# Performance work log

Hardware: AMD Instinct MI355X
Metric: run time of the kernel (lower is better)

Reference implementation:

```python
import jax, jax.numpy as jnp
import numpy as np
from jax import lax

K = 33  # avgpool kernel
P = 16  # padding
EPS = 1e-08


def _box_sum(x):
    # Sum over 33x33 windows, stride 1, zero padding 16 on H and W (NCHW).
    return lax.reduce_window(
        x, 0.0, lax.add,
        window_dimensions=(1, 1, K, K),
        window_strides=(1, 1, 1, 1),
        padding=((0, 0), (0, 0), (P, P), (P, P)),
    )


def setup_inputs() -> dict:
    key = jax.random.key(0)
    input_tensor = jax.random.normal(key, (64, 1, 80, 3000), dtype=jnp.float32)
    return {"input_tensor": input_tensor}


def reference(input_tensor):
    B, C, H, W = input_tensor.shape
    # count_include_pad=False: divide by number of VALID elements per window.
    counts = _box_sum(jnp.ones((1, 1, H, W), dtype=input_tensor.dtype))
    local_mean = _box_sum(input_tensor) / counts
    centered = input_tensor - local_mean
    local_var = _box_sum(centered * centered) / counts
    local_std = jnp.sqrt(local_var)
    return centered / (local_std + EPS)
```

## Files before the change

kernel.cpp:

```cpp
#include <hip/hip_runtime.h>
#include <hip/hip_bf16.h>
#include <math.h>

#define BB 64
#define HH 80
#define WW 3000
#define RAD 16
#define TW 96
#define XSW 68
#define HXS 116
#define NSTRIP 32
#define NT 1024
#define EPSF 1e-8f

#define XS_WORDS (HH * XSW)
#define HXP_OFF  XS_WORDS
#define HXP_WORDS (TW * HXS)
#define ICH_OFF  (XS_WORDS + HXP_WORDS)
#define TOT_WORDS (ICH_OFF + HH)

typedef float f32x2 __attribute__((ext_vector_type(2)));
typedef float f32x4 __attribute__((ext_vector_type(4)));

__device__ __forceinline__ float bflo(uint32_t w) { return __uint_as_float(w << 16); }
__device__ __forceinline__ float bfhi(uint32_t w) { return __uint_as_float(w & 0xffff0000u); }
__device__ __forceinline__ uint32_t packbf2(float lo, float hi) {
    union { __hip_bfloat162 h2; uint32_t u; } u;
    u.h2 = __hip_bfloat162(__float2bfloat16(lo), __float2bfloat16(hi));
    return u.u;
}
__device__ __forceinline__ f32x2 uw(uint32_t w) {
    f32x2 r; r.x = bflo(w); r.y = bfhi(w); return r;
}

#define E4(V, J) ((J) == 0 ? (V).x : ((J) == 1 ? (V).y : ((J) == 2 ? (V).z : (V).w)))
#define W24(Q) E4((Q) < 4 ? v0 : (Q) < 8 ? v1 : (Q) < 12 ? v2 : (Q) < 16 ? v3 : (Q) < 20 ? v4 : v5, (Q) & 3)
#define W48(Q) E4((Q) < 4 ? R0 : (Q) < 8 ? R1 : (Q) < 12 ? R2 : (Q) < 16 ? R3 : (Q) < 20 ? R4 : \
                  (Q) < 24 ? R5 : (Q) < 28 ? R6 : (Q) < 32 ? R7 : (Q) < 36 ? R8 : \
                  (Q) < 40 ? R9 : (Q) < 44 ? R10 : R11, (Q) & 3)
#define F16(K) E4((K) < 4 ? f0 : (K) < 8 ? f1 : (K) < 12 ? f2 : f3, (K) & 3)

__global__ __launch_bounds__(NT, 8)
void localnorm_kernel(const float* __restrict__ in, float* __restrict__ out) {
    extern __shared__ uint32_t smem[];
    uint32_t* Hxp = smem + HXP_OFF;
    float* inv_ch = (float*)(smem + ICH_OFF);

    const int t     = threadIdx.x;
    const int strip = blockIdx.x % NSTRIP;
    const int b     = blockIdx.x / NSTRIP;
    const int c0    = strip * TW;

    if (t < HH) {
        int lo = max(t - RAD, 0), hi = min(t + RAD, HH - 1);
        inv_ch[t] = 1.0f / (float)(hi - lo + 1);
    }
    if (t < 768) {
        const int col = t >> 3;
        const int c8  = t & 7;
        const int off = col * HXS + ((c8 < 4) ? (c8 * 4) : (96 + (c8 - 4) * 4));
        *(uint4*)(Hxp + off) = make_uint4(0u, 0u, 0u, 0u);
    }

    {
        const float* inb = in + (size_t)b * (HH * WW);
        #pragma unroll
        for (int it = 0; it < 3; ++it) {
            const int id = t + it * NT;
            if (it < 2 || id < 2560) {
                const int row = id >> 5;
                const int q   = id & 31;
                const int gc  = c0 - 16 + 4 * q;
                uint2 w2;
                if (gc >= 0 && gc + 4 <= WW) {
                    float4 v = *(const float4*)(inb + (size_t)row * WW + gc);
                    w2.x = packbf2(v.x, v.y);
                    w2.y = packbf2(v.z, v.w);
                } else {
                    float p0 = (gc     >= 0 && gc     < WW) ? inb[(size_t)row * WW + gc]     : 0.f;
                    float p1 = (gc + 1 >= 0 && gc + 1 < WW) ? inb[(size_t)row * WW + gc + 1] : 0.f;
                    float p2 = (gc + 2 >= 0 && gc + 2 < WW) ? inb[(size_t)row * WW + gc + 2] : 0.f;
                    float p3 = (gc + 3 >= 0 && gc + 3 < WW) ? inb[(size_t)row * WW + gc + 3] : 0.f;
                    w2.x = packbf2(p0, p1);
                    w2.y = packbf2(p2, p3);
                }
                *(uint2*)(smem + row * XSW + 2 * q) = w2;
            }
        }
    }
    __syncthreads();

    {
        const int row = t % HH;
        const int s16 = t / HH;
        if (s16 < 6) {
            const uint32_t* xr = smem + row * XSW + s16 * 8;
            uint4 v0 = *(const uint4*)(xr);
            uint4 v1 = *(const uint4*)(xr + 4);
            uint4 v2 = *(const uint4*)(xr + 8);
            uint4 v3 = *(const uint4*)(xr + 12);
            uint4 v4 = *(const uint4*)(xr + 16);
            uint4 v5 = *(const uint4*)(xr + 20);
            float l16 = bflo(W24(16));
            f32x2 pA; pA.x = l16;       pA.y = 0.f;
            f32x2 qA; qA.x = l16 * l16; qA.y = 0.f;
            f32x2 pB; pB.x = 0.f; pB.y = 0.f;
            f32x2 qB; qB.x = 0.f; qB.y = 0.f;
            #pragma unroll
            for (int q = 0; q < 16; q += 2) {
                f32x2 uA = uw(W24(q));
                f32x2 uB = uw(W24(q + 1));
                pA += uA;      pB += uB;
                qA += uA * uA; qB += uB * uB;
            }
            f32x2 ps = pA + pB, qs = qA + qB;
            float ax  = ps.x + ps.y;
            float axx = qs.x + qs.y;
            uint32_t* hw = Hxp + (s16 * 16) * HXS + row + 16;
            #pragma unroll
            for (int k = 0; k < 8; ++k) {
                uint32_t wS = W24(k), wE = W24(k + 16);
                float lS = bflo(wS), hE = bfhi(wE);
                float a1x  = ax - lS + hE;
                float a1xx = axx - lS * lS + hE * hE;
                hw[(2 * k) * HXS]     = packbf2(ax, axx);
                hw[(2 * k + 1) * HXS] = packbf2(a1x, a1xx);
                if (k != 7) {
                    float hS = bfhi(wS), lN = bflo(W24(k + 17));
                    ax  = a1x - hS + lN;
                    axx = a1xx - hS * hS + lN * lN;
                }
            }
        }
    }
    __syncthreads();

    {
        const int c    = t % TW;
        const int band = t / TW;
        const int gc   = c0 + c;
        if (band < 5 && gc < WW) {
            const int r0 = band * 16;
            const uint32_t* hp = Hxp + c * HXS + r0;
            uint4 R0  = *(const uint4*)(hp);
            uint4 R1  = *(const uint4*)(hp + 4);
            uint4 R2  = *(const uint4*)(hp + 8);
            uint4 R3  = *(const uint4*)(hp + 12);
            uint4 R4  = *(const uint4*)(hp + 16);
            uint4 R5  = *(const uint4*)(hp + 20);
            uint4 R6  = *(const uint4*)(hp + 24);
            uint4 R7  = *(const uint4*)(hp + 28);
            uint4 R8  = *(const uint4*)(hp + 32);
            uint4 R9  = *(const uint4*)(hp + 36);
            uint4 R10 = *(const uint4*)(hp + 40);
            uint4 R11 = *(const uint4*)(hp + 44);
            f32x2 aA = uw(W48(32));
            f32x2 aB; aB.x = 0.f; aB.y = 0.f;
            #pragma unroll
            for (int q = 0; q < 32; q += 2) {
                aA += uw(W48(q));
                aB += uw(W48(q + 1));
            }
            f32x2 acc = aA + aB;
            const float icw = 1.0f / (float)(min(gc + RAD, WW - 1) - max(gc - RAD, 0) + 1);
            f32x4 f0 = *(const f32x4*)(inv_ch + r0);
            f32x4 f1 = *(const f32x4*)(inv_ch + r0 + 4);
            f32x4 f2 = *(const f32x4*)(inv_ch + r0 + 8);
            f32x4 f3 = *(const f32x4*)(inv_ch + r0 + 12);
            const int  xwoff  = (c + 16) >> 1;
            const bool hiHf   = ((c + 16) & 1) != 0;
            float* outb = out + (size_t)b * (HH * WW);
            #pragma unroll
            for (int k = 0; k < 16; ++k) {
                const int r = r0 + k;
                const float ninv = F16(k) * icw;
                f32x2 me = acc * ninv;
                float var = fmaxf(me.y - me.x * me.x, 1e-24f);
#if defined(__has_builtin) && __has_builtin(__builtin_amdgcn_rsqf)
                float isd = __builtin_amdgcn_rsqf(var);
#else
                float isd = __builtin_amdgcn_rcpf(__builtin_amdgcn_sqrtf(var) + EPSF);
#endif
                uint32_t xw = smem[r * XSW + xwoff];
                float xv = hiHf ? bfhi(xw) : bflo(xw);
                outb[(size_t)r * WW + gc] = (xv - me.x) * isd;
                if (k != 15) {
                    acc += uw(W48(k + 33)) - uw(W48(k));
                }
            }
        }
    }
}

extern "C" void kernel_launch(void* const* d_in, const int* in_sizes, int n_in,
                              void* d_out, int out_size, void* d_ws, size_t ws_size,
                              hipStream_t stream) {
    const float* in = (const float*)d_in[0];
    float* out = (float*)d_out;

    const size_t lds_bytes = (size_t)TOT_WORDS * sizeof(uint32_t);
    static bool attr_set = false;
    if (!attr_set) {
        (void)hipFuncSetAttribute((const void*)localnorm_kernel,
                                  hipFuncAttributeMaxDynamicSharedMemorySize,
                                  (int)lds_bytes);
        attr_set = true;
    }

    dim3 grid(BB * NSTRIP);
    dim3 block(NT);
    localnorm_kernel<<<grid, block, lds_bytes, stream>>>(in, out);
}
```

Measured before the change: 36.40 us.

## Stage input tile as fp32 via direct global-to-LDS loads with narrower strips

Input is now staged in LDS as fp32 rather than packed bf16, using the global_load_lds builtin so interior strips copy straight from global memory into LDS without passing through registers. The strip width drops from 96 to 80 columns (38 strips), and the horizontal pass is rewritten to work on fp32 values with FMA accumulation. The aim is to cut register round-trips and packing work in the load phase and to improve precision. The cost is a larger LDS footprint per block, more blocks overall, and extra halo reloads from the narrower strips.

```diff
diff --git a/kernel.cpp b/kernel.cpp
--- a/kernel.cpp
+++ b/kernel.cpp
@@ -6,10 +6,11 @@
 #define HH 80
 #define WW 3000
 #define RAD 16
-#define TW 96
-#define XSW 68
+#define TW 80
+#define NLOAD 112
+#define XSW 112
 #define HXS 116
-#define NSTRIP 32
+#define NSTRIP 38
 #define NT 1024
 #define EPSF 1e-8f
 
@@ -33,8 +34,21 @@
     f32x2 r; r.x = bflo(w); r.y = bfhi(w); return r;
 }
 
+#if defined(__has_builtin)
+#if __has_builtin(__builtin_amdgcn_global_load_lds)
+#define HAVE_GLL 1
+__device__ __forceinline__ void gload_lds16(const float* g, float* l) {
+    __builtin_amdgcn_global_load_lds(
+        (const __attribute__((address_space(1))) void*)g,
+        (__attribute__((address_space(3))) void*)l, 16, 0, 0);
+}
+#endif
+#endif
+
 #define E4(V, J) ((J) == 0 ? (V).x : ((J) == 1 ? (V).y : ((J) == 2 ? (V).z : (V).w)))
-#define W24(Q) E4((Q) < 4 ? v0 : (Q) < 8 ? v1 : (Q) < 12 ? v2 : (Q) < 16 ? v3 : (Q) < 20 ? v4 : v5, (Q) & 3)
+#define F48(Q) E4((Q) < 4 ? G0 : (Q) < 8 ? G1 : (Q) < 12 ? G2 : (Q) < 16 ? G3 : (Q) < 20 ? G4 : \
+                  (Q) < 24 ? G5 : (Q) < 28 ? G6 : (Q) < 32 ? G7 : (Q) < 36 ? G8 : \
+                  (Q) < 40 ? G9 : (Q) < 44 ? G10 : G11, (Q) & 3)
 #define W48(Q) E4((Q) < 4 ? R0 : (Q) < 8 ? R1 : (Q) < 12 ? R2 : (Q) < 16 ? R3 : (Q) < 20 ? R4 : \
                   (Q) < 24 ? R5 : (Q) < 28 ? R6 : (Q) < 32 ? R7 : (Q) < 36 ? R8 : \
                   (Q) < 40 ? R9 : (Q) < 44 ? R10 : R11, (Q) & 3)
@@ -43,48 +57,63 @@
 __global__ __launch_bounds__(NT, 8)
 void localnorm_kernel(const float* __restrict__ in, float* __restrict__ out) {
     extern __shared__ uint32_t smem[];
-    uint32_t* Hxp = smem + HXP_OFF;
-    float* inv_ch = (float*)(smem + ICH_OFF);
+    float*    smemf = (float*)smem;
+    uint32_t* Hxp   = smem + HXP_OFF;
+    float*   inv_ch = (float*)(smem + ICH_OFF);
 
     const int t     = threadIdx.x;
     const int strip = blockIdx.x % NSTRIP;
     const int b     = blockIdx.x / NSTRIP;
     const int c0    = strip * TW;
+    const float* inb = in + (size_t)b * (HH * WW);
 
     if (t < HH) {
         int lo = max(t - RAD, 0), hi = min(t + RAD, HH - 1);
         inv_ch[t] = 1.0f / (float)(hi - lo + 1);
     }
-    if (t < 768) {
+    if (t < 640) {
         const int col = t >> 3;
         const int c8  = t & 7;
         const int off = col * HXS + ((c8 < 4) ? (c8 * 4) : (96 + (c8 - 4) * 4));
         *(uint4*)(Hxp + off) = make_uint4(0u, 0u, 0u, 0u);
     }
 
-    {
-        const float* inb = in + (size_t)b * (HH * WW);
+    bool dma = false;
+#ifdef HAVE_GLL
+    dma = (c0 >= 16) && (c0 + NLOAD - 16 <= WW);
+#endif
+    if (dma) {
+#ifdef HAVE_GLL
+        const float* gsrc = inb + (c0 - 16);
+        #pragma unroll
+        for (int i = 0; i < 3; ++i) {
+            const int ck = t + i * NT;
+            if (i < 2 || ck < 2240) {
+                const int row = ck / 28;
+                const int m   = ck - row * 28;
+                gload_lds16(gsrc + (size_t)row * WW + 4 * m, smemf + 4 * ck);
+            }
+        }
+#endif
+    } else {
         #pragma unroll
         for (int it = 0; it < 3; ++it) {
             const int id = t + it * NT;
-            if (it < 2 || id < 2560) {
-                const int row = id >> 5;
-                const int q   = id & 31;
+            if (it < 2 || id < 2240) {
+                const int row = id / 28;
+                const int q   = id - row * 28;
                 const int gc  = c0 - 16 + 4 * q;
-                uint2 w2;
+                const float* rp = inb + (size_t)row * WW;
+                f32x4 v;
                 if (gc >= 0 && gc + 4 <= WW) {
-                    float4 v = *(const float4*)(inb + (size_t)row * WW + gc);
-                    w2.x = packbf2(v.x, v.y);
-                    w2.y = packbf2(v.z, v.w);
+                    v = *(const f32x4*)(rp + gc);
                 } else {
-                    float p0 = (gc     >= 0 && gc     < WW) ? inb[(size_t)row * WW + gc]     : 0.f;
-                    float p1 = (gc + 1 >= 0 && gc + 1 < WW) ? inb[(size_t)row * WW + gc + 1] : 0.f;
-                    float p2 = (gc + 2 >= 0 && gc + 2 < WW) ? inb[(size_t)row * WW + gc + 2] : 0.f;
-                    float p3 = (gc + 3 >= 0 && gc + 3 < WW) ? inb[(size_t)row * WW + gc + 3] : 0.f;
-                    w2.x = packbf2(p0, p1);
-                    w2.y = packbf2(p2, p3);
+                    v.x = (gc     >= 0 && gc     < WW) ? rp[gc]     : 0.f;
+                    v.y = (gc + 1 >= 0 && gc + 1 < WW) ? rp[gc + 1] : 0.f;
+                    v.z = (gc + 2 >= 0 && gc + 2 < WW) ? rp[gc + 2] : 0.f;
+                    v.w = (gc + 3 >= 0 && gc + 3 < WW) ? rp[gc + 3] : 0.f;
                 }
-                *(uint2*)(smem + row * XSW + 2 * q) = w2;
+                *(f32x4*)(smemf + row * XSW + 4 * q) = v;
             }
         }
     }
@@ -92,43 +121,43 @@
 
     {
         const int row = t % HH;
-        const int s16 = t / HH;
-        if (s16 < 6) {
-            const uint32_t* xr = smem + row * XSW + s16 * 8;
-            uint4 v0 = *(const uint4*)(xr);
-            uint4 v1 = *(const uint4*)(xr + 4);
-            uint4 v2 = *(const uint4*)(xr + 8);
-            uint4 v3 = *(const uint4*)(xr + 12);
-            uint4 v4 = *(const uint4*)(xr + 16);
-            uint4 v5 = *(const uint4*)(xr + 20);
-            float l16 = bflo(W24(16));
-            f32x2 pA; pA.x = l16;       pA.y = 0.f;
-            f32x2 qA; qA.x = l16 * l16; qA.y = 0.f;
-            f32x2 pB; pB.x = 0.f; pB.y = 0.f;
-            f32x2 qB; qB.x = 0.f; qB.y = 0.f;
-            #pragma unroll
-            for (int q = 0; q < 16; q += 2) {
-                f32x2 uA = uw(W24(q));
-                f32x2 uB = uw(W24(q + 1));
-                pA += uA;      pB += uB;
-                qA += uA * uA; qB += uB * uB;
-            }
-            f32x2 ps = pA + pB, qs = qA + qB;
-            float ax  = ps.x + ps.y;
-            float axx = qs.x + qs.y;
-            uint32_t* hw = Hxp + (s16 * 16) * HXS + row + 16;
+        const int seg = t / HH;
+        if (seg < 5) {
+            const float* xr = smemf + row * XSW + seg * 16;
+            f32x4 G0  = *(const f32x4*)(xr);
+            f32x4 G1  = *(const f32x4*)(xr + 4);
+            f32x4 G2  = *(const f32x4*)(xr + 8);
+            f32x4 G3  = *(const f32x4*)(xr + 12);
+            f32x4 G4  = *(const f32x4*)(xr + 16);
+            f32x4 G5  = *(const f32x4*)(xr + 20);
+            f32x4 G6  = *(const f32x4*)(xr + 24);
+            f32x4 G7  = *(const f32x4*)(xr + 28);
+            f32x4 G8  = *(const f32x4*)(xr + 32);
+            f32x4 G9  = *(const f32x4*)(xr + 36);
+            f32x4 G10 = *(const f32x4*)(xr + 40);
+            f32x4 G11 = *(const f32x4*)(xr + 44);
+            float e32 = F48(32);
+            float axA = e32, axB = 0.f;
+            float qxA = e32 * e32, qxB = 0.f;
+            #pragma unroll
+            for (int q = 0; q < 32; q += 2) {
+                float fa = F48(q), fb = F48(q + 1);
+                axA += fa;                 axB += fb;
+                qxA = fmaf(fa, fa, qxA);   qxB = fmaf(fb, fb, qxB);
+            }
+            float ax = axA + axB, axx = qxA + qxB;
+            uint32_t* hw = Hxp + (seg * 16) * HXS + row + 16;
             #pragma unroll
             for (int k = 0; k < 8; ++k) {
-                uint32_t wS = W24(k), wE = W24(k + 16);
-                float lS = bflo(wS), hE = bfhi(wE);
-                float a1x  = ax - lS + hE;
-                float a1xx = axx - lS * lS + hE * hE;
+                float fs = F48(2 * k), fe = F48(2 * k + 33);
+                float a1x  = ax - fs + fe;
+                float a1xx = fmaf(fe, fe, fmaf(-fs, fs, axx));
                 hw[(2 * k) * HXS]     = packbf2(ax, axx);
                 hw[(2 * k + 1) * HXS] = packbf2(a1x, a1xx);
                 if (k != 7) {
-                    float hS = bfhi(wS), lN = bflo(W24(k + 17));
-                    ax  = a1x - hS + lN;
-                    axx = a1xx - hS * hS + lN * lN;
+                    float fs2 = F48(2 * k + 1), fe2 = F48(2 * k + 34);
+                    ax  = a1x - fs2 + fe2;
+                    axx = fmaf(fe2, fe2, fmaf(-fs2, fs2, a1xx));
                 }
             }
         }
@@ -167,8 +196,6 @@
             f32x4 f1 = *(const f32x4*)(inv_ch + r0 + 4);
             f32x4 f2 = *(const f32x4*)(inv_ch + r0 + 8);
             f32x4 f3 = *(const f32x4*)(inv_ch + r0 + 12);
-            const int  xwoff  = (c + 16) >> 1;
-            const bool hiHf   = ((c + 16) & 1) != 0;
             float* outb = out + (size_t)b * (HH * WW);
             #pragma unroll
             for (int k = 0; k < 16; ++k) {
@@ -181,8 +208,7 @@
 #else
                 float isd = __builtin_amdgcn_rcpf(__builtin_amdgcn_sqrtf(var) + EPSF);
 #endif
-                uint32_t xw = smem[r * XSW + xwoff];
-                float xv = hiHf ? bfhi(xw) : bflo(xw);
+                float xv = smemf[r * XSW + c + 16];
                 outb[(size_t)r * WW + gc] = (xv - me.x) * isd;
                 if (k != 15) {
                     acc += uw(W48(k + 33)) - uw(W48(k));
```

Result: no change. 35.76 us, median of 2 (-1.7%).
